# Kernel tuning notes

Measured on AMD Instinct MI355X. Metric: run time of the kernel, lower is better.

The kernel has to match this reference:

```python
import jax, jax.numpy as jnp
import numpy as np
from jax import lax

B, N, D, K = 4, 2048, 1024, 16
TAU = 16.0
LN_EPS = 1e-5


def setup_inputs() -> dict:
    key = jax.random.key(0)
    ks = jax.random.split(key, 8)
    x = jax.random.normal(ks[0], (B, N, D), dtype=jnp.float32)
    Wi = jax.random.normal(ks[1], (D, D), dtype=jnp.float32) * 0.02  # i_proj.weight [out,in]
    We = jax.random.normal(ks[2], (K, D), dtype=jnp.float32) * 0.02  # e_proj.weight
    Wf = jax.random.normal(ks[3], (D, D), dtype=jnp.float32) * 0.02  # f_proj.weight
    Ws = jax.random.normal(ks[4], (K, D), dtype=jnp.float32) * 0.02  # s_proj.weight
    gamma = jnp.ones((D,), dtype=jnp.float32)   # LayerNorm weight
    beta = jnp.zeros((D,), dtype=jnp.float32)   # LayerNorm bias
    Wo = jax.random.normal(ks[5], (D, D), dtype=jnp.float32) * 0.02  # o_proj.weight
    return {"x": x, "Wi": Wi, "We": We, "Wf": Wf, "Ws": Ws,
            "gamma": gamma, "beta": beta, "Wo": Wo}


def _forward(x, Wi, We, Wf, Ws, gamma, beta, Wo):
    # Projections (torch Linear: y = x @ W.T)
    i = jnp.einsum('bnd,ed->bne', x, Wi)          # [B,N,D]
    e = jnp.einsum('bnd,kd->bnk', x, We)          # [B,N,K]  (t_type=0: identity transform)
    s = jnp.einsum('bnd,kd->bnk', x, Ws)          # [B,N,K]
    # f_type=2, use_tau: f = exp(logsigmoid(f_proj(x)) / tau), broadcast over k
    f = jnp.exp(jax.nn.log_sigmoid(jnp.einsum('bnd,ed->bne', x, Wf)) / TAU)  # [B,N,D]

    def step(m, inp):
        i_t, e_t, f_t, s_t = inp                  # [B,D],[B,K],[B,D],[B,K]
        m = f_t[:, None, :] * m + e_t[:, :, None] * i_t[:, None, :]  # [B,K,D]
        y_t = jnp.einsum('bk,bkd->bd', s_t, m)
        return m, y_t

    xs = (jnp.swapaxes(i, 0, 1), jnp.swapaxes(e, 0, 1),
          jnp.swapaxes(f, 0, 1), jnp.swapaxes(s, 0, 1))
    m0 = jnp.zeros((B, K, D), dtype=x.dtype)
    _, ys = lax.scan(step, m0, xs)                # [N,B,D]
    y = jnp.swapaxes(ys, 0, 1)                    # [B,N,D]

    # LayerNorm then output projection
    mu = jnp.mean(y, axis=-1, keepdims=True)
    var = jnp.mean((y - mu) ** 2, axis=-1, keepdims=True)
    yn = (y - mu) * lax.rsqrt(var + LN_EPS) * gamma + beta
    return jnp.einsum('bnd,ed->bne', yn, Wo)


def reference(x, Wi, We, Wf, Ws, gamma, beta, Wo):
    return _forward(x, Wi, We, Wf, Ws, gamma, beta, Wo)
```

## Files before the change

### kernel.cpp

```cpp
#include <hip/hip_runtime.h>
#include <hip/hip_bf16.h>
#include <stdint.h>

#define B_ 4
#define N_ 2048
#define D_ 1024
#define K_ 16
#define MROWS (B_*N_)
#define NC_ 64
#define CLEN_ (N_/NC_)

typedef unsigned short u16;
typedef __attribute__((ext_vector_type(8))) short bf16x8;
typedef __attribute__((ext_vector_type(8))) short short8;
typedef __attribute__((ext_vector_type(4))) float f32x4;

__device__ __forceinline__ u16 f2bf(float f) {
  uint32_t u = __float_as_uint(f);
  u = u + 0x7fffu + ((u >> 16) & 1u);
  return (u16)(u >> 16);
}
__device__ __forceinline__ float bf2f(u16 h) {
  uint32_t u = ((uint32_t)h) << 16;
  return __uint_as_float(u);
}
__device__ __forceinline__ float fgate(float z) {
  float ls = (z >= 0.0f) ? -__logf(1.0f + __expf(-z)) : (z - __logf(1.0f + __expf(z)));
  return __expf(ls * 0.0625f);
}

__global__ __launch_bounds__(256) void cast_kernel(const float* __restrict__ in,
                                                   u16* __restrict__ out, int n) {
  int i = (blockIdx.x * 256 + threadIdx.x) * 4;
  if (i >= n) return;
  float4 v = *(const float4*)(in + i);
  ushort4 o;
  o.x = f2bf(v.x); o.y = f2bf(v.y); o.z = f2bf(v.z); o.w = f2bf(v.w);
  *(ushort4*)(out + i) = o;
}

__global__ __launch_bounds__(256) void prep_kernel(const float* __restrict__ Wo,
                                                   const float* __restrict__ gamma,
                                                   const float* __restrict__ beta,
                                                   u16* __restrict__ Wg,
                                                   float* __restrict__ u,
                                                   float* __restrict__ v) {
  __shared__ float red[8];
  int c = blockIdx.x;
  int tid = threadIdx.x;
  int k0 = tid * 4;
  float4 wv = *(const float4*)(Wo + (size_t)c * D_ + k0);
  float4 g4 = *(const float4*)(gamma + k0);
  float4 b4 = *(const float4*)(beta + k0);
  ushort4 o;
  o.x = f2bf(wv.x * g4.x); o.y = f2bf(wv.y * g4.y);
  o.z = f2bf(wv.z * g4.z); o.w = f2bf(wv.w * g4.w);
  *(ushort4*)(Wg + (size_t)c * D_ + k0) = o;
  float us = wv.x * g4.x + wv.y * g4.y + wv.z * g4.z + wv.w * g4.w;
  float vs = wv.x * b4.x + wv.y * b4.y + wv.z * b4.z + wv.w * b4.w;
  for (int off = 32; off > 0; off >>= 1) {
    us += __shfl_xor(us, off);
    vs += __shfl_xor(vs, off);
  }
  int w = tid >> 6, l = tid & 63;
  if (l == 0) { red[w] = us; red[4 + w] = vs; }
  __syncthreads();
  if (tid == 0) {
    u[c] = red[0] + red[1] + red[2] + red[3];
    v[c] = red[4] + red[5] + red[6] + red[7];
  }
}

#define GL_LDS(gp, lp) \
  __builtin_amdgcn_global_load_lds( \
      (const __attribute__((address_space(1))) void*)(gp), \
      (__attribute__((address_space(3))) void*)(lp), 16, 0, 0)

#define WAITVM(n)  asm volatile("s_waitcnt vmcnt(" #n ")" ::: "memory")
#define SCHEDB()   __builtin_amdgcn_sched_barrier(0)

__global__ __launch_bounds__(512, 1) void ring_fused(const u16* __restrict__ A,
                                                     const u16* __restrict__ W0,
                                                     const u16* __restrict__ W1,
                                                     u16* __restrict__ C0,
                                                     u16* __restrict__ C1) {
  __shared__ __align__(16) u16 lds[3 * 24576];

  const int tid = threadIdx.x;
  const int w = tid >> 6, l = tid & 63;
  const int wr = w >> 1, wc = w & 1;

  const int orig = blockIdx.x;
  const int wg = (orig & 7) * 64 + (orig >> 3);
  const int bm = wg / 16;
  const int bn = wg % 16;

  const u16* W;
  u16* C;
  int ncol0;
  if (bn >= 8) { W = W1; C = C1; ncol0 = (bn - 8) * 128; }
  else         { W = W0; C = C0; ncol0 = bn * 128; }

  const int sw = ((l & 7) ^ ((l >> 3) & 7)) * 8;
  const u16* aSrc = A + (size_t)(bm * 256 + w * 8 + (l >> 3)) * 1024 + sw;
  const u16* bSrc = W + (size_t)(ncol0 + w * 8 + (l >> 3)) * 1024 + sw;

#define STAGE_T(t, slot) do { \
    const int _sb = (slot) * 49152 + w * 1024; \
    _Pragma("unroll") \
    for (int j = 0; j < 4; ++j) \
      GL_LDS(aSrc + (size_t)j * 65536 + (t) * 64, (char*)lds + _sb + j * 8192); \
    _Pragma("unroll") \
    for (int j = 0; j < 2; ++j) \
      GL_LDS(bSrc + (size_t)j * 65536 + (t) * 64, (char*)lds + _sb + 32768 + j * 8192); \
  } while (0)

  const int sxe = (l & 7) << 3;
  const int klo = (l >> 4) * 8;
  const int aR0 = (wr * 64 + (l & 15)) * 64;
  const int bR0 = (wc * 64 + (l & 15)) * 64 + 16384;

  f32x4 acc[4][4] = {};

#define COMPUTE(slot) do { \
    const u16* S = lds + (slot) * 24576; \
    bf16x8 b0[4], a0[4], b1[4], a1[4]; \
    _Pragma("unroll") \
    for (int n = 0; n < 4; ++n) b0[n] = *(const bf16x8*)&S[bR0 + n * 1024 + (klo ^ sxe)]; \
    _Pragma("unroll") \
    for (int m = 0; m < 4; ++m) a0[m] = *(const bf16x8*)&S[aR0 + m * 1024 + (klo ^ sxe)]; \
    _Pragma("unroll") \
    for (int n = 0; n < 4; ++n) b1[n] = *(const bf16x8*)&S[bR0 + n * 1024 + ((klo + 32) ^ sxe)]; \
    _Pragma("unroll") \
    for (int m = 0; m < 4; ++m) a1[m] = *(const bf16x8*)&S[aR0 + m * 1024 + ((klo + 32) ^ sxe)]; \
    asm volatile("s_waitcnt lgkmcnt(8)" ::: "memory"); \
    SCHEDB(); \
    __builtin_amdgcn_s_setprio(1); \
    _Pragma("unroll") \
    for (int m = 0; m < 4; ++m) \
      _Pragma("unroll") \
      for (int n = 0; n < 4; ++n) \
        acc[m][n] = __builtin_amdgcn_mfma_f32_16x16x32_bf16(a0[m], b0[n], acc[m][n], 0, 0, 0); \
    __builtin_amdgcn_s_setprio(0); \
    asm volatile("s_waitcnt lgkmcnt(0)" ::: "memory"); \
    SCHEDB(); \
    __builtin_amdgcn_s_setprio(1); \
    _Pragma("unroll") \
    for (int m = 0; m < 4; ++m) \
      _Pragma("unroll") \
      for (int n = 0; n < 4; ++n) \
        acc[m][n] = __builtin_amdgcn_mfma_f32_16x16x32_bf16(a1[m], b1[n], acc[m][n], 0, 0, 0); \
    __builtin_amdgcn_s_setprio(0); \
  } while (0)

  STAGE_T(0, 0);
  STAGE_T(1, 1);
  WAITVM(6);
  __builtin_amdgcn_s_barrier();
  SCHEDB();

#pragma unroll
  for (int t = 0; t < 16; ++t) {
    if (t + 2 < 16) STAGE_T(t + 2, (t + 2) % 3);
    COMPUTE(t % 3);
    if (t < 15) {
      if (t == 14) WAITVM(0);
      else         WAITVM(6);
      __builtin_amdgcn_s_barrier();
      SCHEDB();
    }
  }

  const int orow0 = bm * 256 + wr * 64 + (l >> 4) * 4;
  const int ocol0 = ncol0 + wc * 64 + (l & 15);
#pragma unroll
  for (int m = 0; m < 4; ++m)
#pragma unroll
    for (int n = 0; n < 4; ++n)
#pragma unroll
      for (int r = 0; r < 4; ++r)
        C[(size_t)(orow0 + m * 16 + r) * 1024 + ocol0 + n * 16] = f2bf(acc[m][n][r]);
#undef STAGE_T
#undef COMPUTE
}

__global__ __launch_bounds__(256) void gemm_bt_ln(const u16* __restrict__ A,
                                                  const u16* __restrict__ W,
                                                  float* __restrict__ C,
                                                  const float* __restrict__ rstd,
                                                  const float* __restrict__ mrs,
                                                  const float* __restrict__ u,
                                                  const float* __restrict__ v) {
  __shared__ u16 As[128 * 32];
  __shared__ u16 Bs[128 * 32];
  const int tid = threadIdx.x;
  const int w = tid >> 6, l = tid & 63;
  const int orig = blockIdx.x;
  const int swz = (orig & 7) * 64 + (orig >> 3);
  const int bm = swz >> 3, bn = swz & 7;
  const int wm = (w >> 1) * 64, wn = (w & 1) * 64;
  const int lr = l & 15, lk = (l >> 4) * 8;

  f32x4 acc[4][4] = {};

  for (int kt = 0; kt < 1024; kt += 32) {
#pragma unroll
    for (int j = 0; j < 2; ++j) {
      int ofs = w * 1024 + j * 4096;
      int gofs = ofs + l * 16;
      int row = gofs >> 6;
      int ke = (gofs & 63) >> 1;
      const u16* ga = A + (size_t)(bm * 128 + row) * 1024 + kt + ke;
      const u16* gb = W + (size_t)(bn * 128 + row) * 1024 + kt + ke;
      GL_LDS(ga, (char*)As + ofs);
      GL_LDS(gb, (char*)Bs + ofs);
    }
    __syncthreads();
    bf16x8 af[4], bfr[4];
#pragma unroll
    for (int i2 = 0; i2 < 4; ++i2) {
      af[i2]  = *(const bf16x8*)&As[(wm + i2 * 16 + lr) * 32 + lk];
      bfr[i2] = *(const bf16x8*)&Bs[(wn + i2 * 16 + lr) * 32 + lk];
    }
#pragma unroll
    for (int i2 = 0; i2 < 4; ++i2)
#pragma unroll
      for (int j2 = 0; j2 < 4; ++j2)
        acc[i2][j2] = __builtin_amdgcn_mfma_f32_16x16x32_bf16(af[i2], bfr[j2], acc[i2][j2], 0, 0, 0);
    __syncthreads();
  }

  const int orow0 = bm * 128 + wm + (l >> 4) * 4;
  const int ocol0 = bn * 128 + wn + (l & 15);
#pragma unroll
  for (int i2 = 0; i2 < 4; ++i2) {
#pragma unroll
    for (int j2 = 0; j2 < 4; ++j2) {
      int col = ocol0 + j2 * 16;
      float uc = u[col], vc = v[col];
#pragma unroll
      for (int r = 0; r < 4; ++r) {
        int row = orow0 + i2 * 16 + r;
        C[(size_t)row * 1024 + col] = rstd[row] * acc[i2][j2][r] + mrs[row] * uc + vc;
      }
    }
  }
}

__global__ __launch_bounds__(256) void es_mfma(const u16* __restrict__ xb,
                                               const float* __restrict__ We,
                                               const float* __restrict__ Ws,
                                               float* __restrict__ e,
                                               float* __restrict__ s) {
  __shared__ __align__(16) u16 Bsm[32 * 1024];
  __shared__ __align__(16) u16 Asl[2][64 * 128];

  const int tid = threadIdx.x;
  const int w = tid >> 6, l = tid & 63;
  const int bm = blockIdx.x;

#pragma unroll
  for (int q = 0; q < 16; ++q) {
    int g = q * 256 + tid;
    int n = g >> 7;
    int c = g & 127;
    const float* src = (n < 16 ? We + (size_t)n * 1024 : Ws + (size_t)(n - 16) * 1024) + c * 8;
    float4 v0 = *(const float4*)(src);
    float4 v1 = *(const float4*)(src + 4);
    short8 o;
    o[0] = (short)f2bf(v0.x); o[1] = (short)f2bf(v0.y);
    o[2] = (short)f2bf(v0.z); o[3] = (short)f2bf(v0.w);
    o[4] = (short)f2bf(v1.x); o[5] = (short)f2bf(v1.y);
    o[6] = (short)f2bf(v1.z); o[7] = (short)f2bf(v1.w);
    *(short8*)&Bsm[(size_t)n * 1024 + (size_t)(c ^ (n & 15)) * 8] = o;
  }

  const int arow_par = w * 4 + (l >> 4);
  const int csrc = (l & 15) ^ arow_par;

#define ESTAGE(t, buf) do { \
    _Pragma("unroll") \
    for (int j = 0; j < 4; ++j) { \
      const u16* gp = xb + (size_t)(bm * 64 + j * 16 + arow_par) * 1024 + (t) * 128 + csrc * 8; \
      GL_LDS(gp, (char*)&Asl[(buf)][0] + j * 4096 + w * 1024); \
    } \
  } while (0)

  f32x4 acc[2] = {};

  ESTAGE(0, 0);
  __syncthreads();

#pragma unroll
  for (int t = 0; t < 8; ++t) {
    if (t) { WAITVM(0); __builtin_amdgcn_s_barrier(); }
    if (t + 1 < 8) ESTAGE(t + 1, (t + 1) & 1);
    const int buf = t & 1;
#pragma unroll
    for (int ks = 0; ks < 4; ++ks) {
      bf16x8 af = *(const bf16x8*)&Asl[buf][(size_t)(w * 16 + (l & 15)) * 128 +
                                           (size_t)(((ks * 4 + (l >> 4)) ^ (l & 15))) * 8];
      bf16x8 b0 = *(const bf16x8*)&Bsm[(size_t)(0 + (l & 15)) * 1024 +
                                       (size_t)(((t * 16 + ks * 4 + (l >> 4)) ^ (l & 15))) * 8];
      bf16x8 b1 = *(const bf16x8*)&Bsm[(size_t)(16 + (l & 15)) * 1024 +
                                       (size_t)(((t * 16 + ks * 4 + (l >> 4)) ^ (l & 15))) * 8];
      acc[0] = __builtin_amdgcn_mfma_f32_16x16x32_bf16(af, b0, acc[0], 0, 0, 0);
      acc[1] = __builtin_amdgcn_mfma_f32_16x16x32_bf16(af, b1, acc[1], 0, 0, 0);
    }
  }

  const int orow = bm * 64 + w * 16 + (l >> 4) * 4;
  const int ocol = l & 15;
#pragma unroll
  for (int r = 0; r < 4; ++r) {
    e[(size_t)(orow + r) * K_ + ocol] = acc[0][r];
    s[(size_t)(orow + r) * K_ + ocol] = acc[1][r];
  }
#undef ESTAGE
}

__global__ __launch_bounds__(256, 4) void scan_pass1(const u16* __restrict__ ibb,
                                                     const u16* __restrict__ zbb,
                                                     const float* __restrict__ ebuf,
                                                     float* __restrict__ Asc,
                                                     float* __restrict__ Psc) {
  __shared__ float els[CLEN_ * K_];
  int bid = blockIdx.x;
  int dq = bid & 3, c = (bid >> 2) % NC_, b = bid / (NC_ * 4);
  int d = dq * 256 + threadIdx.x;
  int t0 = c * CLEN_;

  if (threadIdx.x < CLEN_ * K_ / 4) {
    *(float4*)&els[threadIdx.x * 4] =
        *(const float4*)(ebuf + ((size_t)b * N_ + t0) * K_ + threadIdx.x * 4);
  }
  __syncthreads();

  float m[K_];
#pragma unroll
  for (int k = 0; k < K_; ++k) m[k] = 0.f;
  float p = 1.0f;
  const u16* ip = ibb + ((size_t)b * N_ + t0) * D_ + d;
  const u16* zp = zbb + ((size_t)b * N_ + t0) * D_ + d;

#pragma unroll 1
  for (int tb = 0; tb < CLEN_; tb += 8) {
    float iv[8], zv[8];
#pragma unroll
    for (int j = 0; j < 8; ++j) iv[j] = bf2f(ip[(size_t)(tb + j) * D_]);
#pragma unroll
    for (int j = 0; j < 8; ++j) zv[j] = bf2f(zp[(size_t)(tb + j) * D_]);
#pragma unroll
    for (int j = 0; j < 8; ++j) {
      float ft = fgate(zv[j]);
      p *= ft;
      const float* ec = &els[(tb + j) * K_];
#pragma unroll
      for (int k = 0; k < K_; ++k) m[k] = ft * m[k] + ec[k] * iv[j];
    }
  }

  float* ap = Asc + (((size_t)b * NC_ + c) * K_) * D_ + d;
#pragma unroll
  for (int k = 0; k < K_; ++k) ap[(size_t)k * D_] = m[k];
  Psc[((size_t)b * NC_ + c) * D_ + d] = p;
}

__global__ __launch_bounds__(256, 4) void scan_pass2(float* __restrict__ Asc,
                                                     const float* __restrict__ Psc) {
  int idx = blockIdx.x * 256 + threadIdx.x;
  int d = idx & (D_ - 1);
  int k = (idx >> 10) & (K_ - 1);
  int b = idx >> 14;
  float M = 0.f;
#pragma unroll 1
  for (int cb = 0; cb < NC_; cb += 8) {
    float a[8], pp[8];
#pragma unroll
    for (int j = 0; j < 8; ++j) {
      size_t base = (((size_t)b * NC_ + cb + j) * K_ + k) * D_ + d;
      a[j] = Asc[base];
      pp[j] = Psc[((size_t)b * NC_ + cb + j) * D_ + d];
    }
#pragma unroll
    for (int j = 0; j < 8; ++j) {
      size_t base = (((size_t)b * NC_ + cb + j) * K_ + k) * D_ + d;
      Asc[base] = M;
      M = pp[j] * M + a[j];
    }
  }
}

__global__ __launch_bounds__(256, 4) void scan_pass3(const u16* __restrict__ ibb,
                                                     const u16* __restrict__ zbb,
                                                     const float* __restrict__ ebuf,
                                                     const float* __restrict__ sbuf,
                                                     const float* __restrict__ Ssc,
                                                     u16* __restrict__ ybb) {
  __shared__ float els[CLEN_ * K_];
  __shared__ float sls[CLEN_ * K_];
  int bid = blockIdx.x;
  int dq = bid & 3, c = (bid >> 2) % NC_, b = bid / (NC_ * 4);
  int d = dq * 256 + threadIdx.x;
  int t0 = c * CLEN_;

  if (threadIdx.x < CLEN_ * K_ / 4) {
    *(float4*)&els[threadIdx.x * 4] =
        *(const float4*)(ebuf + ((size_t)b * N_ + t0) * K_ + threadIdx.x * 4);
  } else if (threadIdx.x < CLEN_ * K_ / 2) {
    int q = threadIdx.x - CLEN_ * K_ / 4;
    *(float4*)&sls[q * 4] =
        *(const float4*)(sbuf + ((size_t)b * N_ + t0) * K_ + q * 4);
  }

  float m[K_];
  const float* sp0 = Ssc + (((size_t)b * NC_ + c) * K_) * D_ + d;
#pragma unroll
  for (int k = 0; k < K_; ++k) m[k] = sp0[(size_t)k * D_];
  __syncthreads();

  const u16* ip = ibb + ((size_t)b * N_ + t0) * D_ + d;
  const u16* zp = zbb + ((size_t)b * N_ + t0) * D_ + d;
  u16* yp = ybb + ((size_t)b * N_ + t0) * D_ + d;

#pragma unroll 1
  for (int tb = 0; tb < CLEN_; tb += 8) {
    float iv[8], zv[8];
#pragma unroll
    for (int j = 0; j < 8; ++j) iv[j] = bf2f(ip[(size_t)(tb + j) * D_]);
#pragma unroll
    for (int j = 0; j < 8; ++j) zv[j] = bf2f(zp[(size_t)(tb + j) * D_]);
#pragma unroll
    for (int j = 0; j < 8; ++j) {
      float ft = fgate(zv[j]);
      const float* ec = &els[(tb + j) * K_];
      const float* sc = &sls[(tb + j) * K_];
      float y = 0.f;
#pragma unroll
      for (int k = 0; k < K_; ++k) {
        m[k] = ft * m[k] + ec[k] * iv[j];
        y += sc[k] * m[k];
      }
      yp[(size_t)(tb + j) * D_] = f2bf(y);
    }
  }
}

__global__ __launch_bounds__(256) void rowstat(const u16* __restrict__ y,
                                               float* __restrict__ rstd,
                                               float* __restrict__ mrs) {
  int row = blockIdx.x * 4 + (threadIdx.x >> 6);
  int l = threadIdx.x & 63;
  const u16* yr = y + (size_t)row * D_;
  float sum = 0.f, sq = 0.f;
#pragma unroll
  for (int j = 0; j < 2; ++j) {
    short8 raw = *(const short8*)(yr + l * 16 + j * 8);
#pragma unroll
    for (int q = 0; q < 8; ++q) {
      float f = bf2f((u16)raw[q]);
      sum += f;
      sq += f * f;
    }
  }
  for (int off = 32; off > 0; off >>= 1) {
    sum += __shfl_xor(sum, off);
    sq  += __shfl_xor(sq, off);
  }
  if (l == 0) {
    float mu = sum * (1.0f / D_);
    float var = sq * (1.0f / D_) - mu * mu;
    float rs = rsqrtf(var + 1e-5f);
    rstd[row] = rs;
    mrs[row] = -mu * rs;
  }
}

extern "C" void kernel_launch(void* const* d_in, const int* in_sizes, int n_in,
                              void* d_out, int out_size, void* d_ws, size_t ws_size,
                              hipStream_t stream) {
  const float* x     = (const float*)d_in[0];
  const float* Wi    = (const float*)d_in[1];
  const float* We    = (const float*)d_in[2];
  const float* Wf    = (const float*)d_in[3];
  const float* Ws    = (const float*)d_in[4];
  const float* gamma = (const float*)d_in[5];
  const float* beta  = (const float*)d_in[6];
  const float* Wo    = (const float*)d_in[7];
  float* out = (float*)d_out;

  char* p = (char*)d_ws;
  u16* xb   = (u16*)p;  p += (size_t)MROWS * D_ * 2;
  u16* wib  = (u16*)p;  p += (size_t)D_ * D_ * 2;
  u16* wfb  = (u16*)p;  p += (size_t)D_ * D_ * 2;
  u16* wgb  = (u16*)p;  p += (size_t)D_ * D_ * 2;
  u16* ibb  = (u16*)p;  p += (size_t)MROWS * D_ * 2;
  u16* zbb  = (u16*)p;  p += (size_t)MROWS * D_ * 2;
  u16* ybb  = (u16*)p;  p += (size_t)MROWS * D_ * 2;
  float* ebuf = (float*)p; p += (size_t)MROWS * K_ * 4;
  float* sbuf = (float*)p; p += (size_t)MROWS * K_ * 4;
  float* Asc  = (float*)p; p += (size_t)B_ * NC_ * K_ * D_ * 4;
  float* Psc  = (float*)p; p += (size_t)B_ * NC_ * D_ * 4;
  float* rstd = (float*)p; p += (size_t)MROWS * 4;
  float* mrs  = (float*)p; p += (size_t)MROWS * 4;
  float* ub   = (float*)p; p += (size_t)D_ * 4;
  float* vb   = (float*)p; p += (size_t)D_ * 4;

  cast_kernel<<<MROWS * D_ / 1024, 256, 0, stream>>>(x, xb, MROWS * D_);
  cast_kernel<<<D_ * D_ / 1024, 256, 0, stream>>>(Wi, wib, D_ * D_);
  cast_kernel<<<D_ * D_ / 1024, 256, 0, stream>>>(Wf, wfb, D_ * D_);
  prep_kernel<<<D_, 256, 0, stream>>>(Wo, gamma, beta, wgb, ub, vb);

  ring_fused<<<512, 512, 0, stream>>>(xb, wib, wfb, ibb, zbb);

  es_mfma<<<MROWS / 64, 256, 0, stream>>>(xb, We, Ws, ebuf, sbuf);

  scan_pass1<<<B_ * NC_ * 4, 256, 0, stream>>>(ibb, zbb, ebuf, Asc, Psc);
  scan_pass2<<<B_ * K_ * D_ / 256, 256, 0, stream>>>(Asc, Psc);
  scan_pass3<<<B_ * NC_ * 4, 256, 0, stream>>>(ibb, zbb, ebuf, sbuf, Asc, ybb);

  rowstat<<<MROWS / 4, 256, 0, stream>>>(ybb, rstd, mrs);

  gemm_bt_ln<<<512, 256, 0, stream>>>(ybb, wgb, out, rstd, mrs, ub, vb);
}
```

Measured before the change: 166.8 us.

## Fuse gate into GEMM epilogue, interleave i/f buffers, double scan chunks

The projection GEMM epilogue now computes the forget gate directly and writes i and (1-f) interleaved into one buffer. The scan passes therefore read one 32-bit word per timestep instead of two 16-bit loads and no longer evaluate exp/log per element. Storing 1-f in bf16 is meant to keep precision for f values near 1. The chunk count goes from 64 to 128, which raises scan parallelism but makes pass2 and the carry buffers larger. LDS reads of e and s are vectorised as float4.

```diff
diff --git a/kernel.cpp b/kernel.cpp
--- a/kernel.cpp
+++ b/kernel.cpp
@@ -7,7 +7,7 @@
 #define D_ 1024
 #define K_ 16
 #define MROWS (B_*N_)
-#define NC_ 64
+#define NC_ 128
 #define CLEN_ (N_/NC_)
 
 typedef unsigned short u16;
@@ -82,8 +82,7 @@
 __global__ __launch_bounds__(512, 1) void ring_fused(const u16* __restrict__ A,
                                                      const u16* __restrict__ W0,
                                                      const u16* __restrict__ W1,
-                                                     u16* __restrict__ C0,
-                                                     u16* __restrict__ C1) {
+                                                     u16* __restrict__ izb) {
   __shared__ __align__(16) u16 lds[3 * 24576];
 
   const int tid = threadIdx.x;
@@ -96,10 +95,9 @@
   const int bn = wg % 16;
 
   const u16* W;
-  u16* C;
-  int ncol0;
-  if (bn >= 8) { W = W1; C = C1; ncol0 = (bn - 8) * 128; }
-  else         { W = W0; C = C0; ncol0 = bn * 128; }
+  int ncol0, sel;
+  if (bn >= 8) { W = W1; sel = 1; ncol0 = (bn - 8) * 128; }
+  else         { W = W0; sel = 0; ncol0 = bn * 128; }
 
   const int sw = ((l & 7) ^ ((l >> 3) & 7)) * 8;
   const u16* aSrc = A + (size_t)(bm * 256 + w * 8 + (l >> 3)) * 1024 + sw;
@@ -178,8 +176,13 @@
 #pragma unroll
     for (int n = 0; n < 4; ++n)
 #pragma unroll
-      for (int r = 0; r < 4; ++r)
-        C[(size_t)(orow0 + m * 16 + r) * 1024 + ocol0 + n * 16] = f2bf(acc[m][n][r]);
+      for (int r = 0; r < 4; ++r) {
+        int row = orow0 + m * 16 + r;
+        int col = ocol0 + n * 16;
+        float v = acc[m][n][r];
+        if (sel) v = 1.0f - fgate(v);
+        izb[2 * ((size_t)row * 1024 + col) + sel] = f2bf(v);
+      }
 #undef STAGE_T
 #undef COMPUTE
 }
@@ -319,8 +322,7 @@
 #undef ESTAGE
 }
 
-__global__ __launch_bounds__(256, 4) void scan_pass1(const u16* __restrict__ ibb,
-                                                     const u16* __restrict__ zbb,
+__global__ __launch_bounds__(256, 4) void scan_pass1(const u16* __restrict__ izb,
                                                      const float* __restrict__ ebuf,
                                                      float* __restrict__ Asc,
                                                      float* __restrict__ Psc) {
@@ -340,23 +342,29 @@
 #pragma unroll
   for (int k = 0; k < K_; ++k) m[k] = 0.f;
   float p = 1.0f;
-  const u16* ip = ibb + ((size_t)b * N_ + t0) * D_ + d;
-  const u16* zp = zbb + ((size_t)b * N_ + t0) * D_ + d;
+  const u16* ip = izb + 2 * (((size_t)b * N_ + t0) * D_ + d);
 
 #pragma unroll 1
   for (int tb = 0; tb < CLEN_; tb += 8) {
-    float iv[8], zv[8];
-#pragma unroll
-    for (int j = 0; j < 8; ++j) iv[j] = bf2f(ip[(size_t)(tb + j) * D_]);
-#pragma unroll
-    for (int j = 0; j < 8; ++j) zv[j] = bf2f(zp[(size_t)(tb + j) * D_]);
+    uint32_t uv[8];
+#pragma unroll
+    for (int j = 0; j < 8; ++j)
+      uv[j] = *(const uint32_t*)(ip + 2 * (size_t)(tb + j) * D_);
 #pragma unroll
     for (int j = 0; j < 8; ++j) {
-      float ft = fgate(zv[j]);
+      float it = bf2f((u16)(uv[j] & 0xffffu));
+      float ft = 1.0f - bf2f((u16)(uv[j] >> 16));
       p *= ft;
-      const float* ec = &els[(tb + j) * K_];
-#pragma unroll
-      for (int k = 0; k < K_; ++k) m[k] = ft * m[k] + ec[k] * iv[j];
+      const float4* e4 = (const float4*)&els[(tb + j) * K_];
+      float4 ea = e4[0], eb = e4[1], ec2 = e4[2], ed = e4[3];
+      m[0] = ft * m[0] + ea.x * it;  m[1] = ft * m[1] + ea.y * it;
+      m[2] = ft * m[2] + ea.z * it;  m[3] = ft * m[3] + ea.w * it;
+      m[4] = ft * m[4] + eb.x * it;  m[5] = ft * m[5] + eb.y * it;
+      m[6] = ft * m[6] + eb.z * it;  m[7] = ft * m[7] + eb.w * it;
+      m[8] = ft * m[8] + ec2.x * it; m[9] = ft * m[9] + ec2.y * it;
+      m[10] = ft * m[10] + ec2.z * it; m[11] = ft * m[11] + ec2.w * it;
+      m[12] = ft * m[12] + ed.x * it;  m[13] = ft * m[13] + ed.y * it;
+      m[14] = ft * m[14] + ed.z * it;  m[15] = ft * m[15] + ed.w * it;
     }
   }
 
@@ -391,8 +399,7 @@
   }
 }
 
-__global__ __launch_bounds__(256, 4) void scan_pass3(const u16* __restrict__ ibb,
-                                                     const u16* __restrict__ zbb,
+__global__ __launch_bounds__(256, 4) void scan_pass3(const u16* __restrict__ izb,
                                                      const float* __restrict__ ebuf,
                                                      const float* __restrict__ sbuf,
                                                      const float* __restrict__ Ssc,
@@ -419,28 +426,40 @@
   for (int k = 0; k < K_; ++k) m[k] = sp0[(size_t)k * D_];
   __syncthreads();
 
-  const u16* ip = ibb + ((size_t)b * N_ + t0) * D_ + d;
-  const u16* zp = zbb + ((size_t)b * N_ + t0) * D_ + d;
+  const u16* ip = izb + 2 * (((size_t)b * N_ + t0) * D_ + d);
   u16* yp = ybb + ((size_t)b * N_ + t0) * D_ + d;
 
 #pragma unroll 1
   for (int tb = 0; tb < CLEN_; tb += 8) {
-    float iv[8], zv[8];
-#pragma unroll
-    for (int j = 0; j < 8; ++j) iv[j] = bf2f(ip[(size_t)(tb + j) * D_]);
-#pragma unroll
-    for (int j = 0; j < 8; ++j) zv[j] = bf2f(zp[(size_t)(tb + j) * D_]);
+    uint32_t uv[8];
+#pragma unroll
+    for (int j = 0; j < 8; ++j)
+      uv[j] = *(const uint32_t*)(ip + 2 * (size_t)(tb + j) * D_);
 #pragma unroll
     for (int j = 0; j < 8; ++j) {
-      float ft = fgate(zv[j]);
-      const float* ec = &els[(tb + j) * K_];
-      const float* sc = &sls[(tb + j) * K_];
+      float it = bf2f((u16)(uv[j] & 0xffffu));
+      float ft = 1.0f - bf2f((u16)(uv[j] >> 16));
+      const float4* e4 = (const float4*)&els[(tb + j) * K_];
+      const float4* s4 = (const float4*)&sls[(tb + j) * K_];
+      float4 ea = e4[0], eb = e4[1], ec2 = e4[2], ed = e4[3];
+      float4 sa = s4[0], sb = s4[1], sc2 = s4[2], sd = s4[3];
       float y = 0.f;
-#pragma unroll
-      for (int k = 0; k < K_; ++k) {
-        m[k] = ft * m[k] + ec[k] * iv[j];
-        y += sc[k] * m[k];
-      }
+      m[0] = ft * m[0] + ea.x * it;  y += sa.x * m[0];
+      m[1] = ft * m[1] + ea.y * it;  y += sa.y * m[1];
+      m[2] = ft * m[2] + ea.z * it;  y += sa.z * m[2];
+      m[3] = ft * m[3] + ea.w * it;  y += sa.w * m[3];
+      m[4] = ft * m[4] + eb.x * it;  y += sb.x * m[4];
+      m[5] = ft * m[5] + eb.y * it;  y += sb.y * m[5];
+      m[6] = ft * m[6] + eb.z * it;  y += sb.z * m[6];
+      m[7] = ft * m[7] + eb.w * it;  y += sb.w * m[7];
+      m[8] = ft * m[8] + ec2.x * it; y += sc2.x * m[8];
+      m[9] = ft * m[9] + ec2.y * it; y += sc2.y * m[9];
+      m[10] = ft * m[10] + ec2.z * it; y += sc2.z * m[10];
+      m[11] = ft * m[11] + ec2.w * it; y += sc2.w * m[11];
+      m[12] = ft * m[12] + ed.x * it;  y += sd.x * m[12];
+      m[13] = ft * m[13] + ed.y * it;  y += sd.y * m[13];
+      m[14] = ft * m[14] + ed.z * it;  y += sd.z * m[14];
+      m[15] = ft * m[15] + ed.w * it;  y += sd.w * m[15];
       yp[(size_t)(tb + j) * D_] = f2bf(y);
     }
   }
@@ -494,8 +513,7 @@
   u16* wib  = (u16*)p;  p += (size_t)D_ * D_ * 2;
   u16* wfb  = (u16*)p;  p += (size_t)D_ * D_ * 2;
   u16* wgb  = (u16*)p;  p += (size_t)D_ * D_ * 2;
-  u16* ibb  = (u16*)p;  p += (size_t)MROWS * D_ * 2;
-  u16* zbb  = (u16*)p;  p += (size_t)MROWS * D_ * 2;
+  u16* izb  = (u16*)p;  p += (size_t)MROWS * D_ * 4;
   u16* ybb  = (u16*)p;  p += (size_t)MROWS * D_ * 2;
   float* ebuf = (float*)p; p += (size_t)MROWS * K_ * 4;
   float* sbuf = (float*)p; p += (size_t)MROWS * K_ * 4;
@@ -511,13 +529,13 @@
   cast_kernel<<<D_ * D_ / 1024, 256, 0, stream>>>(Wf, wfb, D_ * D_);
   prep_kernel<<<D_, 256, 0, stream>>>(Wo, gamma, beta, wgb, ub, vb);
 
-  ring_fused<<<512, 512, 0, stream>>>(xb, wib, wfb, ibb, zbb);
+  ring_fused<<<512, 512, 0, stream>>>(xb, wib, wfb, izb);
 
   es_mfma<<<MROWS / 64, 256, 0, stream>>>(xb, We, Ws, ebuf, sbuf);
 
-  scan_pass1<<<B_ * NC_ * 4, 256, 0, stream>>>(ibb, zbb, ebuf, Asc, Psc);
+  scan_pass1<<<B_ * NC_ * 4, 256, 0, stream>>>(izb, ebuf, Asc, Psc);
   scan_pass2<<<B_ * K_ * D_ / 256, 256, 0, stream>>>(Asc, Psc);
-  scan_pass3<<<B_ * NC_ * 4, 256, 0, stream>>>(ibb, zbb, ebuf, sbuf, Asc, ybb);
+  scan_pass3<<<B_ * NC_ * 4, 256, 0, stream>>>(izb, ebuf, sbuf, Asc, ybb);
 
   rowstat<<<MROWS / 4, 256, 0, stream>>>(ybb, rstd, mrs);
 
```

Result: slower. 202.3 us (+21.3%).
